# Kernel tuning notes

Hardware: AMD Instinct MI355X
Metric: run time of the kernel (lower is better)

## Reference

```python
import jax, jax.numpy as jnp
import numpy as np

EMBED_DIM = 1024
NUM_HEADS = 16
HEAD_DIM = EMBED_DIM // NUM_HEADS


def setup_inputs() -> dict:
    key = jax.random.key(0)
    ks = jax.random.split(key, 5)
    B, S, D = 2, 2048, EMBED_DIM
    scale_w = 1.0 / np.sqrt(D)
    x = jax.random.normal(ks[0], (B, S, D), dtype=jnp.float32)
    Wq = jax.random.normal(ks[1], (D, D), dtype=jnp.float32) * scale_w
    Wk = jax.random.normal(ks[2], (D, D), dtype=jnp.float32) * scale_w
    Wv = jax.random.normal(ks[3], (D, D), dtype=jnp.float32) * scale_w
    Wo = jax.random.normal(ks[4], (D, D), dtype=jnp.float32) * scale_w
    return {"x": x, "Wq": Wq, "Wk": Wk, "Wv": Wv, "Wo": Wo}


def reference(x, Wq, Wk, Wv, Wo):
    B, S, D = x.shape
    H, Dh = NUM_HEADS, HEAD_DIM
    scale = 1.0 / jnp.sqrt(jnp.asarray(Dh, dtype=x.dtype))

    def split_heads(t):
        return t.reshape(B, S, H, Dh).transpose(0, 2, 1, 3)  # [B,H,S,Dh]

    q = split_heads(x @ Wq)
    k = split_heads(x @ Wk)
    v = split_heads(x @ Wv)

    scores = jnp.einsum("bhqd,bhkd->bhqk", q, k) * scale
    causal = jnp.tril(jnp.ones((S, S), dtype=bool))[None, None]
    scores = jnp.where(causal, scores, jnp.asarray(-1e9, dtype=scores.dtype))
    weights = jax.nn.softmax(scores, axis=-1)
    attn = jnp.einsum("bhqk,bhkd->bhqd", weights, v)
    attn = attn.transpose(0, 2, 1, 3).reshape(B, S, D)
    return attn @ Wo
```

## Files before the change

### kernel.cpp

```cpp
#include <hip/hip_runtime.h>
#include <cstdint>

typedef __bf16 bf16;
typedef __bf16 bf16x2 __attribute__((ext_vector_type(2)));
typedef __bf16 bf16x4 __attribute__((ext_vector_type(4)));
typedef __bf16 bf16x8 __attribute__((ext_vector_type(8)));
typedef float f32x4 __attribute__((ext_vector_type(4)));

constexpr int S = 2048, D = 1024, H = 16, HD = 64, B = 2;
constexpr size_t TSZ = (size_t)B * H * S * HD;

__device__ __forceinline__ f32x4 mfma16(bf16x8 a, bf16x8 b, f32x4 c) {
  return __builtin_amdgcn_mfma_f32_16x16x32_bf16(a, b, c, 0, 0, 0);
}

__device__ __forceinline__ void gl_lds16(const bf16* g, bf16* s) {
  __builtin_amdgcn_global_load_lds((__attribute__((address_space(1))) void*)g,
                                   (__attribute__((address_space(3))) void*)s,
                                   16, 0, 0);
}

__global__ __launch_bounds__(256) void prep_x(const float* __restrict__ x,
                                              bf16* __restrict__ xb) {
  const size_t i = (size_t)blockIdx.x * 256 + threadIdx.x;
  const float4 a = ((const float4*)x)[2 * i];
  const float4 b = ((const float4*)x)[2 * i + 1];
  bf16x8 o = {(bf16)a.x, (bf16)a.y, (bf16)a.z, (bf16)a.w,
              (bf16)b.x, (bf16)b.y, (bf16)b.z, (bf16)b.w};
  *(bf16x8*)&xb[i * 8] = o;
}

__global__ __launch_bounds__(256) void prep_w(const float* __restrict__ W0,
                                              const float* __restrict__ W1,
                                              const float* __restrict__ W2,
                                              const float* __restrict__ W3,
                                              bf16* __restrict__ Wt) {
  __shared__ __align__(16) bf16 Lt[64][68];
  const int z = blockIdx.z;
  const float* W = z == 0 ? W0 : z == 1 ? W1 : z == 2 ? W2 : W3;
  const int k0 = blockIdx.x * 64, n0 = blockIdx.y * 64;
  const int t = threadIdx.x, tr = t >> 4, tc = (t & 15) * 4;
#pragma unroll
  for (int p = 0; p < 4; ++p) {
    const int r = 16 * p + tr;
    const float4 v = *(const float4*)&W[(size_t)(k0 + r) * D + n0 + tc];
    Lt[tc + 0][r] = (bf16)v.x;
    Lt[tc + 1][r] = (bf16)v.y;
    Lt[tc + 2][r] = (bf16)v.z;
    Lt[tc + 3][r] = (bf16)v.w;
  }
  __syncthreads();
#pragma unroll
  for (int p = 0; p < 4; ++p) {
    const int n = 16 * p + tr;
    const bf16x4 o = *(const bf16x4*)&Lt[n][tc];
    *(bf16x4*)&Wt[((size_t)z * D + n0 + n) * D + k0 + tc] = o;
  }
}

template <int MODE>
__global__ __launch_bounds__(256) void gemm_bt(const bf16* __restrict__ A,
                                               const bf16* __restrict__ Bt,
                                               void* __restrict__ Cp) {
  constexpr int K = 1024;
  __shared__ __align__(16) bf16 As[128 * 64];
  __shared__ __align__(16) bf16 Bs[128 * 64];

  const int bid = blockIdx.x, nwg = gridDim.x;
  const int lg = (bid & 7) * (nwg >> 3) + (bid >> 3);
  const int bm = (lg & 31) * 128;
  const int bn = (lg >> 5) * 128;

  const int t = threadIdx.x, l = t & 63, w = t >> 6;
  const int c = l & 15, g = l >> 4, cx = c & 7;
  const int lrow = l >> 3;
  const int srcc = ((l & 7) ^ lrow) << 3;
  const int wm = (w >> 1) * 64, wn = (w & 1) * 64;

  f32x4 acc[4][4] = {};

  for (int kt = 0; kt < K / 64; ++kt) {
    const int k0 = kt * 64;
    __syncthreads();
#pragma unroll
    for (int i = 0; i < 4; ++i) {
      const int ci = i * 4 + w;
      const int row = ci * 8 + lrow;
      gl_lds16(A + (size_t)(bm + row) * K + k0 + srcc, As + ci * 512 + l * 8);
      gl_lds16(Bt + (size_t)(bn + row) * K + k0 + srcc, Bs + ci * 512 + l * 8);
    }
    __syncthreads();

    bf16x8 af[4][2], bfv[4][2];
#pragma unroll
    for (int mi = 0; mi < 4; ++mi) {
      const int row = wm + mi * 16 + c;
#pragma unroll
      for (int kh = 0; kh < 2; ++kh)
        af[mi][kh] = *(const bf16x8*)&As[row * 64 + (((kh * 4 + g) ^ cx) << 3)];
    }
#pragma unroll
    for (int ni = 0; ni < 4; ++ni) {
      const int row = wn + ni * 16 + c;
#pragma unroll
      for (int kh = 0; kh < 2; ++kh)
        bfv[ni][kh] = *(const bf16x8*)&Bs[row * 64 + (((kh * 4 + g) ^ cx) << 3)];
    }
#pragma unroll
    for (int mi = 0; mi < 4; ++mi)
#pragma unroll
      for (int ni = 0; ni < 4; ++ni) {
        acc[mi][ni] = mfma16(af[mi][0], bfv[ni][0], acc[mi][ni]);
        acc[mi][ni] = mfma16(af[mi][1], bfv[ni][1], acc[mi][ni]);
      }
  }

#pragma unroll
  for (int mi = 0; mi < 4; ++mi)
#pragma unroll
    for (int ni = 0; ni < 4; ++ni)
#pragma unroll
      for (int r = 0; r < 4; ++r) {
        const int m = bm + wm + mi * 16 + 4 * g + r;
        const int n = bn + wn + ni * 16 + c;
        const float v = acc[mi][ni][r];
        if constexpr (MODE == 0) {
          const int which = n >> 10, nn = n & 1023;
          const int h = nn >> 6, d = nn & 63;
          const int bb = m >> 11, s = m & 2047;
          ((bf16*)Cp)[which * TSZ + ((((size_t)bb * H + h) * S + s) << 6) + d] =
              (bf16)v;
        } else {
          ((float*)Cp)[(size_t)m * D + n] = v;
        }
      }
}

__global__ __launch_bounds__(256, 4) void attn3(const bf16* __restrict__ Q,
                                                const bf16* __restrict__ Kg,
                                                const bf16* __restrict__ Vg,
                                                bf16* __restrict__ O) {
  __shared__ __align__(16) bf16 Ks[64 * 64];
  __shared__ __align__(16) bf16 Vt[64 * 64];
  __shared__ __align__(16) bf16 Pb[4][16 * 64];

  const int bid = blockIdx.x;
  const int qt = 31 - (bid >> 5);
  const int bh = bid & 31;
  const int t = threadIdx.x, l = t & 63, w = t >> 6;
  const int c = l & 15, g = l >> 4, cx = c & 7;
  const int bb = bh >> 4, h = bh & 15;
  const float SC = 0.18033688011112042f;
  const float THRS = 44.3614195558365f;

  const bf16* Kbase = Kg + (size_t)bh * S * HD;
  const bf16* Vbase = Vg + (size_t)bh * S * HD;

  const int q0 = qt * 64;
  const int qglob = q0 + 16 * w + c;
  const bf16* Qrow = Q + ((size_t)bh * S + qglob) * HD;
  const bf16x8 qf0 = *(const bf16x8*)&Qrow[g * 8];
  const bf16x8 qf1 = *(const bf16x8*)&Qrow[32 + g * 8];

  const int kv0 = t >> 3, dg0 = t & 7;
  const int kv1 = kv0 + 32;
  const int p2 = t & 31, dgv = t >> 5;

  bf16x8 ka0 = *(const bf16x8*)&Kbase[kv0 * 64 + dg0 * 8];
  bf16x8 ka1 = *(const bf16x8*)&Kbase[kv1 * 64 + dg0 * 8];
  bf16x8 va0 = *(const bf16x8*)&Vbase[(2 * p2) * 64 + dgv * 8];
  bf16x8 va1 = *(const bf16x8*)&Vbase[(2 * p2 + 1) * 64 + dgv * 8];

  f32x4 oacc[4] = {};
  float mrun = -1e30f, lrun = 0.f;

  for (int kt = 0; kt <= qt; ++kt) {
    __syncthreads();
    *(bf16x8*)&Ks[kv0 * 64 + ((dg0 ^ (kv0 & 7)) << 3)] = ka0;
    *(bf16x8*)&Ks[kv1 * 64 + ((dg0 ^ (kv1 & 7)) << 3)] = ka1;
#pragma unroll
    for (int i = 0; i < 8; ++i) {
      const int vd = 8 * dgv + i;
      bf16x2 pr2 = {va0[i], va1[i]};
      *(bf16x2*)&Vt[vd * 64 + (((p2 >> 2) ^ i) << 3) + ((p2 & 3) << 1)] = pr2;
    }
    bf16x8 kn0 = ka0, kn1 = ka1, vn0 = va0, vn1 = va1;
    if (kt < qt) {
      const bf16* Kt = Kbase + (size_t)(kt + 1) * 64 * HD;
      const bf16* Vs = Vbase + (size_t)(kt + 1) * 64 * HD;
      kn0 = *(const bf16x8*)&Kt[kv0 * 64 + dg0 * 8];
      kn1 = *(const bf16x8*)&Kt[kv1 * 64 + dg0 * 8];
      vn0 = *(const bf16x8*)&Vs[(2 * p2) * 64 + dgv * 8];
      vn1 = *(const bf16x8*)&Vs[(2 * p2 + 1) * 64 + dgv * 8];
    }
    __syncthreads();

    f32x4 st[4];
    __builtin_amdgcn_s_setprio(1);
#pragma unroll
    for (int ct = 0; ct < 4; ++ct) {
      const int krow = ct * 16 + c;
      const bf16x8 kf0 = *(const bf16x8*)&Ks[krow * 64 + ((g ^ cx) << 3)];
      const bf16x8 kf1 = *(const bf16x8*)&Ks[krow * 64 + (((4 + g) ^ cx) << 3)];
      f32x4 z = {};
      z = mfma16(kf0, qf0, z);
      st[ct] = mfma16(kf1, qf1, z);
    }
    __builtin_amdgcn_s_setprio(0);

    if (kt == qt) {
#pragma unroll
      for (int ct = 0; ct < 4; ++ct)
#pragma unroll
        for (int r = 0; r < 4; ++r)
          if (kt * 64 + ct * 16 + 4 * g + r > qglob) st[ct][r] = -1e30f;
    }

    float mt = st[0][0];
#pragma unroll
    for (int ct = 0; ct < 4; ++ct)
#pragma unroll
      for (int r = 0; r < 4; ++r) mt = fmaxf(mt, st[ct][r]);
    mt = fmaxf(mt, __shfl_xor(mt, 16));
    mt = fmaxf(mt, __shfl_xor(mt, 32));
    if (!__all(mt <= mrun + THRS)) {
      const float mnew = fmaxf(mrun, mt);
      const float fac = __builtin_amdgcn_exp2f((mrun - mnew) * SC);
      lrun *= fac;
#pragma unroll
      for (int ct = 0; ct < 4; ++ct)
#pragma unroll
        for (int r = 0; r < 4; ++r) oacc[ct][r] *= fac;
      mrun = mnew;
    }
    float p[4][4];
    float ps = 0.f;
#pragma unroll
    for (int ct = 0; ct < 4; ++ct)
#pragma unroll
      for (int r = 0; r < 4; ++r) {
        p[ct][r] = __builtin_amdgcn_exp2f((st[ct][r] - mrun) * SC);
        ps += p[ct][r];
      }
    ps += __shfl_xor(ps, 16);
    ps += __shfl_xor(ps, 32);
    lrun += ps;

    bf16* Pw = &Pb[w][0];
#pragma unroll
    for (int ct = 0; ct < 4; ++ct)
#pragma unroll
      for (int pr = 0; pr < 2; ++pr) {
        const int ch = (2 * ct + (g >> 1)) ^ cx;
        bf16x2 pk = {(bf16)p[ct][2 * pr], (bf16)p[ct][2 * pr + 1]};
        *(bf16x2*)&Pw[c * 64 + ch * 8 + (g & 1) * 4 + pr * 2] = pk;
      }
    const bf16x8 pa0 = *(const bf16x8*)&Pw[c * 64 + ((g ^ cx) << 3)];
    const bf16x8 pa1 = *(const bf16x8*)&Pw[c * 64 + (((4 + g) ^ cx) << 3)];

    __builtin_amdgcn_s_setprio(1);
#pragma unroll
    for (int ct = 0; ct < 4; ++ct) {
      const int vrow = ct * 16 + c;
      const bf16x8 vt0 = *(const bf16x8*)&Vt[vrow * 64 + ((g ^ cx) << 3)];
      const bf16x8 vt1 = *(const bf16x8*)&Vt[vrow * 64 + (((4 + g) ^ cx) << 3)];
      oacc[ct] = mfma16(vt0, pa0, oacc[ct]);
      oacc[ct] = mfma16(vt1, pa1, oacc[ct]);
    }
    __builtin_amdgcn_s_setprio(0);

    ka0 = kn0; ka1 = kn1; va0 = vn0; va1 = vn1;
  }

  const float inv = 1.f / lrun;
  bf16* Orow = O + ((size_t)bb * S + qglob) * D + h * 64;
#pragma unroll
  for (int ct = 0; ct < 4; ++ct)
#pragma unroll
    for (int pr = 0; pr < 2; ++pr) {
      bf16x2 pk = {(bf16)(oacc[ct][2 * pr] * inv),
                   (bf16)(oacc[ct][2 * pr + 1] * inv)};
      *(bf16x2*)&Orow[ct * 16 + 4 * g + 2 * pr] = pk;
    }
}

extern "C" void kernel_launch(void* const* d_in, const int* in_sizes, int n_in,
                              void* d_out, int out_size, void* d_ws, size_t ws_size,
                              hipStream_t stream) {
  const float* x  = (const float*)d_in[0];
  const float* Wq = (const float*)d_in[1];
  const float* Wk = (const float*)d_in[2];
  const float* Wv = (const float*)d_in[3];
  const float* Wo = (const float*)d_in[4];
  float* out = (float*)d_out;

  bf16* xb  = (bf16*)d_ws;
  bf16* Wt  = xb + (size_t)B * S * D;
  bf16* QKV = Wt + (size_t)4 * D * D;
  bf16* Ab  = QKV + 3 * TSZ;

  prep_x<<<2048, 256, 0, stream>>>(x, xb);
  prep_w<<<dim3(16, 16, 4), 256, 0, stream>>>(Wq, Wk, Wv, Wo, Wt);
  gemm_bt<0><<<768, 256, 0, stream>>>(xb, Wt, QKV);
  attn3<<<1024, 256, 0, stream>>>(QKV, QKV + TSZ, QKV + 2 * TSZ, Ab);
  gemm_bt<1><<<256, 256, 0, stream>>>(Ab, Wt + (size_t)3 * D * D, out);
}
```

Before: 109.2 us.

## Split KV across wave pairs with paired causal tiles and in-register P

The attention kernel now uses 32-row query tiles, each processed by two head-wave pairs that split every 64-key tile in half, then merges the two partial softmax states through shared memory. Each block handles a short and a long query tile (qp and 63-qp) so causal work per block is balanced. The P fragment is built directly in registers as the MFMA operand, removing the per-wave P staging in shared memory, and V is read with a transposed half-tile layout. The trade-off is an extra LDS merge, two more barriers per phase, and K/V tiles being reloaded for each of the two phases.

```diff
diff --git a/kernel.cpp b/kernel.cpp
--- a/kernel.cpp
+++ b/kernel.cpp
@@ -136,18 +136,19 @@
       }
 }
 
-__global__ __launch_bounds__(256, 4) void attn3(const bf16* __restrict__ Q,
+__global__ __launch_bounds__(256, 4) void attn5(const bf16* __restrict__ Q,
                                                 const bf16* __restrict__ Kg,
                                                 const bf16* __restrict__ Vg,
                                                 bf16* __restrict__ O) {
-  __shared__ __align__(16) bf16 Ks[64 * 64];
-  __shared__ __align__(16) bf16 Vt[64 * 64];
-  __shared__ __align__(16) bf16 Pb[4][16 * 64];
+  __shared__ __align__(16) unsigned char shraw[17408];
+  bf16* Ks = (bf16*)shraw;
+  bf16* Vt = (bf16*)(shraw + 8192);
+  float* X = (float*)shraw;
 
   const int bid = blockIdx.x;
-  const int qt = 31 - (bid >> 5);
-  const int bh = bid & 31;
+  const int qp = bid >> 5, bh = bid & 31;
   const int t = threadIdx.x, l = t & 63, w = t >> 6;
+  const int h2 = w >> 1, pk = w & 1;
   const int c = l & 15, g = l >> 4, cx = c & 7;
   const int bb = bh >> 4, h = bh & 15;
   const float SC = 0.18033688011112042f;
@@ -156,132 +157,139 @@
   const bf16* Kbase = Kg + (size_t)bh * S * HD;
   const bf16* Vbase = Vg + (size_t)bh * S * HD;
 
-  const int q0 = qt * 64;
-  const int qglob = q0 + 16 * w + c;
-  const bf16* Qrow = Q + ((size_t)bh * S + qglob) * HD;
-  const bf16x8 qf0 = *(const bf16x8*)&Qrow[g * 8];
-  const bf16x8 qf1 = *(const bf16x8*)&Qrow[32 + g * 8];
-
-  const int kv0 = t >> 3, dg0 = t & 7;
-  const int kv1 = kv0 + 32;
+  const int kv0 = t >> 3, dg0 = t & 7, kv1 = kv0 + 32;
   const int p2 = t & 31, dgv = t >> 5;
 
-  bf16x8 ka0 = *(const bf16x8*)&Kbase[kv0 * 64 + dg0 * 8];
-  bf16x8 ka1 = *(const bf16x8*)&Kbase[kv1 * 64 + dg0 * 8];
-  bf16x8 va0 = *(const bf16x8*)&Vbase[(2 * p2) * 64 + dgv * 8];
-  bf16x8 va1 = *(const bf16x8*)&Vbase[(2 * p2 + 1) * 64 + dgv * 8];
-
-  f32x4 oacc[4] = {};
-  float mrun = -1e30f, lrun = 0.f;
-
-  for (int kt = 0; kt <= qt; ++kt) {
+  for (int ph = 0; ph < 2; ++ph) {
+    const int qt = ph ? (63 - qp) : qp;
+    const int nT = (qt >> 1) + 1;
+    const int qglob = qt * 32 + 16 * h2 + c;
+
+    const bf16* Qrow = Q + ((size_t)bh * S + qglob) * HD;
+    const bf16x8 qf0 = *(const bf16x8*)&Qrow[g * 8];
+    const bf16x8 qf1 = *(const bf16x8*)&Qrow[32 + g * 8];
+
+    bf16x8 ka0 = *(const bf16x8*)&Kbase[kv0 * 64 + dg0 * 8];
+    bf16x8 ka1 = *(const bf16x8*)&Kbase[kv1 * 64 + dg0 * 8];
+    bf16x8 va0 = *(const bf16x8*)&Vbase[(2 * p2) * 64 + dgv * 8];
+    bf16x8 va1 = *(const bf16x8*)&Vbase[(2 * p2 + 1) * 64 + dgv * 8];
+
+    f32x4 oacc[4] = {};
+    float mrun = -1e30f, lrun = 0.f;
+
+    for (int kt = 0; kt < nT; ++kt) {
+      __syncthreads();
+      *(bf16x8*)&Ks[kv0 * 64 + ((dg0 ^ (kv0 & 7)) << 3)] = ka0;
+      *(bf16x8*)&Ks[kv1 * 64 + ((dg0 ^ (kv1 & 7)) << 3)] = ka1;
+#pragma unroll
+      for (int i = 0; i < 8; ++i) {
+        const int vd = 8 * dgv + i;
+        bf16x2 pr2 = {va0[i], va1[i]};
+        *(bf16x2*)&Vt[vd * 64 + (((p2 >> 2) ^ i) << 3) + ((p2 & 3) << 1)] = pr2;
+      }
+      if (kt + 1 < nT) {
+        const bf16* Kt = Kbase + (size_t)(kt + 1) * 64 * HD;
+        const bf16* Vs = Vbase + (size_t)(kt + 1) * 64 * HD;
+        ka0 = *(const bf16x8*)&Kt[kv0 * 64 + dg0 * 8];
+        ka1 = *(const bf16x8*)&Kt[kv1 * 64 + dg0 * 8];
+        va0 = *(const bf16x8*)&Vs[(2 * p2) * 64 + dgv * 8];
+        va1 = *(const bf16x8*)&Vs[(2 * p2 + 1) * 64 + dgv * 8];
+      }
+      __syncthreads();
+
+      f32x4 st[2];
+      __builtin_amdgcn_s_setprio(1);
+#pragma unroll
+      for (int ct = 0; ct < 2; ++ct) {
+        const int krow = 32 * pk + 16 * ct + c;
+        const bf16x8 kf0 = *(const bf16x8*)&Ks[krow * 64 + ((g ^ cx) << 3)];
+        const bf16x8 kf1 = *(const bf16x8*)&Ks[krow * 64 + (((4 + g) ^ cx) << 3)];
+        f32x4 z = {};
+        z = mfma16(kf0, qf0, z);
+        st[ct] = mfma16(kf1, qf1, z);
+      }
+      __builtin_amdgcn_s_setprio(0);
+
+      if (kt == nT - 1) {
+#pragma unroll
+        for (int ct = 0; ct < 2; ++ct)
+#pragma unroll
+          for (int r = 0; r < 4; ++r)
+            if (kt * 64 + 32 * pk + 16 * ct + 4 * g + r > qglob)
+              st[ct][r] = -3e38f;
+      }
+
+      float mt = st[0][0];
+#pragma unroll
+      for (int ct = 0; ct < 2; ++ct)
+#pragma unroll
+        for (int r = 0; r < 4; ++r) mt = fmaxf(mt, st[ct][r]);
+      mt = fmaxf(mt, __shfl_xor(mt, 16));
+      mt = fmaxf(mt, __shfl_xor(mt, 32));
+      if (!__all(mt <= mrun + THRS)) {
+        const float mnew = fmaxf(mrun, mt);
+        const float fac = __builtin_amdgcn_exp2f((mrun - mnew) * SC);
+        lrun *= fac;
+#pragma unroll
+        for (int q = 0; q < 4; ++q)
+#pragma unroll
+          for (int r = 0; r < 4; ++r) oacc[q][r] *= fac;
+        mrun = mnew;
+      }
+      float p[2][4];
+      float ps = 0.f;
+#pragma unroll
+      for (int ct = 0; ct < 2; ++ct)
+#pragma unroll
+        for (int r = 0; r < 4; ++r) {
+          p[ct][r] = __builtin_amdgcn_exp2f((st[ct][r] - mrun) * SC);
+          ps += p[ct][r];
+        }
+      ps += __shfl_xor(ps, 16);
+      ps += __shfl_xor(ps, 32);
+      lrun += ps;
+
+      const bf16x8 pa = {(bf16)p[0][0], (bf16)p[0][1], (bf16)p[0][2], (bf16)p[0][3],
+                         (bf16)p[1][0], (bf16)p[1][1], (bf16)p[1][2], (bf16)p[1][3]};
+
+      __builtin_amdgcn_s_setprio(1);
+#pragma unroll
+      for (int cp = 0; cp < 4; ++cp) {
+        const int vb = (16 * cp + c) * 64;
+        const bf16x4 lo = *(const bf16x4*)&Vt[vb + ((((pk << 2) + (g >> 1)) ^ cx) << 3) + ((g & 1) << 2)];
+        const bf16x4 hi = *(const bf16x4*)&Vt[vb + ((((pk << 2) + 2 + (g >> 1)) ^ cx) << 3) + ((g & 1) << 2)];
+        const bf16x8 vf = {lo[0], lo[1], lo[2], lo[3], hi[0], hi[1], hi[2], hi[3]};
+        oacc[cp] = mfma16(vf, pa, oacc[cp]);
+      }
+      __builtin_amdgcn_s_setprio(0);
+    }
+
     __syncthreads();
-    *(bf16x8*)&Ks[kv0 * 64 + ((dg0 ^ (kv0 & 7)) << 3)] = ka0;
-    *(bf16x8*)&Ks[kv1 * 64 + ((dg0 ^ (kv1 & 7)) << 3)] = ka1;
-#pragma unroll
-    for (int i = 0; i < 8; ++i) {
-      const int vd = 8 * dgv + i;
-      bf16x2 pr2 = {va0[i], va1[i]};
-      *(bf16x2*)&Vt[vd * 64 + (((p2 >> 2) ^ i) << 3) + ((p2 & 3) << 1)] = pr2;
-    }
-    bf16x8 kn0 = ka0, kn1 = ka1, vn0 = va0, vn1 = va1;
-    if (kt < qt) {
-      const bf16* Kt = Kbase + (size_t)(kt + 1) * 64 * HD;
-      const bf16* Vs = Vbase + (size_t)(kt + 1) * 64 * HD;
-      kn0 = *(const bf16x8*)&Kt[kv0 * 64 + dg0 * 8];
-      kn1 = *(const bf16x8*)&Kt[kv1 * 64 + dg0 * 8];
-      vn0 = *(const bf16x8*)&Vs[(2 * p2) * 64 + dgv * 8];
-      vn1 = *(const bf16x8*)&Vs[(2 * p2 + 1) * 64 + dgv * 8];
-    }
+    float* Xw = X + w * (16 * 68);
+#pragma unroll
+    for (int cp = 0; cp < 4; ++cp)
+      *(f32x4*)&Xw[c * 68 + 16 * cp + 4 * g] = oacc[cp];
+    if (g == 0) { Xw[c * 68 + 64] = mrun; Xw[c * 68 + 65] = lrun; }
     __syncthreads();
-
-    f32x4 st[4];
-    __builtin_amdgcn_s_setprio(1);
-#pragma unroll
-    for (int ct = 0; ct < 4; ++ct) {
-      const int krow = ct * 16 + c;
-      const bf16x8 kf0 = *(const bf16x8*)&Ks[krow * 64 + ((g ^ cx) << 3)];
-      const bf16x8 kf1 = *(const bf16x8*)&Ks[krow * 64 + (((4 + g) ^ cx) << 3)];
-      f32x4 z = {};
-      z = mfma16(kf0, qf0, z);
-      st[ct] = mfma16(kf1, qf1, z);
-    }
-    __builtin_amdgcn_s_setprio(0);
-
-    if (kt == qt) {
-#pragma unroll
-      for (int ct = 0; ct < 4; ++ct)
-#pragma unroll
-        for (int r = 0; r < 4; ++r)
-          if (kt * 64 + ct * 16 + 4 * g + r > qglob) st[ct][r] = -1e30f;
-    }
-
-    float mt = st[0][0];
-#pragma unroll
-    for (int ct = 0; ct < 4; ++ct)
-#pragma unroll
-      for (int r = 0; r < 4; ++r) mt = fmaxf(mt, st[ct][r]);
-    mt = fmaxf(mt, __shfl_xor(mt, 16));
-    mt = fmaxf(mt, __shfl_xor(mt, 32));
-    if (!__all(mt <= mrun + THRS)) {
-      const float mnew = fmaxf(mrun, mt);
-      const float fac = __builtin_amdgcn_exp2f((mrun - mnew) * SC);
-      lrun *= fac;
-#pragma unroll
-      for (int ct = 0; ct < 4; ++ct)
-#pragma unroll
-        for (int r = 0; r < 4; ++r) oacc[ct][r] *= fac;
-      mrun = mnew;
-    }
-    float p[4][4];
-    float ps = 0.f;
-#pragma unroll
-    for (int ct = 0; ct < 4; ++ct)
-#pragma unroll
-      for (int r = 0; r < 4; ++r) {
-        p[ct][r] = __builtin_amdgcn_exp2f((st[ct][r] - mrun) * SC);
-        ps += p[ct][r];
-      }
-    ps += __shfl_xor(ps, 16);
-    ps += __shfl_xor(ps, 32);
-    lrun += ps;
-
-    bf16* Pw = &Pb[w][0];
-#pragma unroll
-    for (int ct = 0; ct < 4; ++ct)
+    const float* Xp = X + (w ^ 1) * (16 * 68);
+    const float m2 = Xp[c * 68 + 64], l2 = Xp[c * 68 + 65];
+    const float mn = fmaxf(mrun, m2);
+    const float f1 = __builtin_amdgcn_exp2f((mrun - mn) * SC);
+    const float f2 = __builtin_amdgcn_exp2f((m2 - mn) * SC);
+    const float linv = 1.f / (lrun * f1 + l2 * f2);
+    bf16* Orow = O + ((size_t)bb * S + qglob) * D + h * 64;
+#pragma unroll
+    for (int j = 0; j < 2; ++j) {
+      const int cp = 2 * pk + j;
+      const f32x4 o2 = *(const f32x4*)&Xp[c * 68 + 16 * cp + 4 * g];
 #pragma unroll
       for (int pr = 0; pr < 2; ++pr) {
-        const int ch = (2 * ct + (g >> 1)) ^ cx;
-        bf16x2 pk = {(bf16)p[ct][2 * pr], (bf16)p[ct][2 * pr + 1]};
-        *(bf16x2*)&Pw[c * 64 + ch * 8 + (g & 1) * 4 + pr * 2] = pk;
-      }
-    const bf16x8 pa0 = *(const bf16x8*)&Pw[c * 64 + ((g ^ cx) << 3)];
-    const bf16x8 pa1 = *(const bf16x8*)&Pw[c * 64 + (((4 + g) ^ cx) << 3)];
-
-    __builtin_amdgcn_s_setprio(1);
-#pragma unroll
-    for (int ct = 0; ct < 4; ++ct) {
-      const int vrow = ct * 16 + c;
-      const bf16x8 vt0 = *(const bf16x8*)&Vt[vrow * 64 + ((g ^ cx) << 3)];
-      const bf16x8 vt1 = *(const bf16x8*)&Vt[vrow * 64 + (((4 + g) ^ cx) << 3)];
-      oacc[ct] = mfma16(vt0, pa0, oacc[ct]);
-      oacc[ct] = mfma16(vt1, pa1, oacc[ct]);
-    }
-    __builtin_amdgcn_s_setprio(0);
-
-    ka0 = kn0; ka1 = kn1; va0 = vn0; va1 = vn1;
+        bf16x2 pkk = {(bf16)((oacc[cp][2 * pr] * f1 + o2[2 * pr] * f2) * linv),
+                      (bf16)((oacc[cp][2 * pr + 1] * f1 + o2[2 * pr + 1] * f2) * linv)};
+        *(bf16x2*)&Orow[16 * cp + 4 * g + 2 * pr] = pkk;
+      }
+    }
   }
-
-  const float inv = 1.f / lrun;
-  bf16* Orow = O + ((size_t)bb * S + qglob) * D + h * 64;
-#pragma unroll
-  for (int ct = 0; ct < 4; ++ct)
-#pragma unroll
-    for (int pr = 0; pr < 2; ++pr) {
-      bf16x2 pk = {(bf16)(oacc[ct][2 * pr] * inv),
-                   (bf16)(oacc[ct][2 * pr + 1] * inv)};
-      *(bf16x2*)&Orow[ct * 16 + 4 * g + 2 * pr] = pk;
-    }
 }
 
 extern "C" void kernel_launch(void* const* d_in, const int* in_sizes, int n_in,
@@ -302,6 +310,6 @@
   prep_x<<<2048, 256, 0, stream>>>(x, xb);
   prep_w<<<dim3(16, 16, 4), 256, 0, stream>>>(Wq, Wk, Wv, Wo, Wt);
   gemm_bt<0><<<768, 256, 0, stream>>>(xb, Wt, QKV);
-  attn3<<<1024, 256, 0, stream>>>(QKV, QKV + TSZ, QKV + 2 * TSZ, Ab);
+  attn5<<<1024, 256, 0, stream>>>(QKV, QKV + TSZ, QKV + 2 * TSZ, Ab);
   gemm_bt<1><<<256, 256, 0, stream>>>(Ab, Wt + (size_t)3 * D * D, out);
 }
```

After: 120.9 us. 1.11x slower.

## Split long causal attention rows across KV halves with a separate merge kernel

Applied to the files above, without the earlier changes.

Query tiles 16-31, which have the longest causal KV ranges, are each split into two blocks that process halves of the KV range. Each block writes unnormalized fp32 partial outputs plus running max and sum to a workspace. A new merge kernel combines the partials and normalizes into the bf16 attention buffer. The launch bound also rises to 6 blocks per CU. The aim is to balance per-block work and raise occupancy, at the cost of an extra kernel launch and fp32 partial-result traffic.

```diff
diff --git a/kernel.cpp b/kernel.cpp
--- a/kernel.cpp
+++ b/kernel.cpp
@@ -136,20 +136,23 @@
       }
 }
 
-__global__ __launch_bounds__(256, 4) void attn3(const bf16* __restrict__ Q,
+__global__ __launch_bounds__(256, 6) void attn6(const bf16* __restrict__ Q,
                                                 const bf16* __restrict__ Kg,
                                                 const bf16* __restrict__ Vg,
-                                                bf16* __restrict__ O) {
+                                                float* __restrict__ Pp) {
   __shared__ __align__(16) bf16 Ks[64 * 64];
   __shared__ __align__(16) bf16 Vt[64 * 64];
   __shared__ __align__(16) bf16 Pb[4][16 * 64];
 
   const int bid = blockIdx.x;
-  const int qt = 31 - (bid >> 5);
-  const int bh = bid & 31;
+  const int bh = bid & 31, e = bid >> 5;
+  int qt, kvA, kvB, half;
+  if (e < 16)      { qt = 31 - e; half = 0; kvA = 0;             kvB = (qt + 2) >> 1; }
+  else if (e < 32) { qt = 47 - e; half = 1; kvA = (qt + 2) >> 1; kvB = qt + 1; }
+  else             { qt = 47 - e; half = 0; kvA = 0;             kvB = qt + 1; }
+
   const int t = threadIdx.x, l = t & 63, w = t >> 6;
   const int c = l & 15, g = l >> 4, cx = c & 7;
-  const int bb = bh >> 4, h = bh & 15;
   const float SC = 0.18033688011112042f;
   const float THRS = 44.3614195558365f;
 
@@ -166,15 +169,17 @@
   const int kv1 = kv0 + 32;
   const int p2 = t & 31, dgv = t >> 5;
 
-  bf16x8 ka0 = *(const bf16x8*)&Kbase[kv0 * 64 + dg0 * 8];
-  bf16x8 ka1 = *(const bf16x8*)&Kbase[kv1 * 64 + dg0 * 8];
-  bf16x8 va0 = *(const bf16x8*)&Vbase[(2 * p2) * 64 + dgv * 8];
-  bf16x8 va1 = *(const bf16x8*)&Vbase[(2 * p2 + 1) * 64 + dgv * 8];
+  const bf16* K0 = Kbase + (size_t)kvA * 64 * HD;
+  const bf16* V0 = Vbase + (size_t)kvA * 64 * HD;
+  bf16x8 ka0 = *(const bf16x8*)&K0[kv0 * 64 + dg0 * 8];
+  bf16x8 ka1 = *(const bf16x8*)&K0[kv1 * 64 + dg0 * 8];
+  bf16x8 va0 = *(const bf16x8*)&V0[(2 * p2) * 64 + dgv * 8];
+  bf16x8 va1 = *(const bf16x8*)&V0[(2 * p2 + 1) * 64 + dgv * 8];
 
   f32x4 oacc[4] = {};
   float mrun = -1e30f, lrun = 0.f;
 
-  for (int kt = 0; kt <= qt; ++kt) {
+  for (int kt = kvA; kt < kvB; ++kt) {
     __syncthreads();
     *(bf16x8*)&Ks[kv0 * 64 + ((dg0 ^ (kv0 & 7)) << 3)] = ka0;
     *(bf16x8*)&Ks[kv1 * 64 + ((dg0 ^ (kv1 & 7)) << 3)] = ka1;
@@ -185,7 +190,7 @@
       *(bf16x2*)&Vt[vd * 64 + (((p2 >> 2) ^ i) << 3) + ((p2 & 3) << 1)] = pr2;
     }
     bf16x8 kn0 = ka0, kn1 = ka1, vn0 = va0, vn1 = va1;
-    if (kt < qt) {
+    if (kt + 1 < kvB) {
       const bf16* Kt = Kbase + (size_t)(kt + 1) * 64 * HD;
       const bf16* Vs = Vbase + (size_t)(kt + 1) * 64 * HD;
       kn0 = *(const bf16x8*)&Kt[kv0 * 64 + dg0 * 8];
@@ -272,16 +277,33 @@
     ka0 = kn0; ka1 = kn1; va0 = vn0; va1 = vn1;
   }
 
-  const float inv = 1.f / lrun;
-  bf16* Orow = O + ((size_t)bb * S + qglob) * D + h * 64;
+  float* Pr = Pp + ((((size_t)bh * 32 + qt) * 2 + half) * 64 + 16 * w + c) * 68;
 #pragma unroll
   for (int ct = 0; ct < 4; ++ct)
-#pragma unroll
-    for (int pr = 0; pr < 2; ++pr) {
-      bf16x2 pk = {(bf16)(oacc[ct][2 * pr] * inv),
-                   (bf16)(oacc[ct][2 * pr + 1] * inv)};
-      *(bf16x2*)&Orow[ct * 16 + 4 * g + 2 * pr] = pk;
-    }
+    *(f32x4*)&Pr[16 * ct + 4 * g] = oacc[ct];
+  if (g == 0) { Pr[64] = mrun; Pr[65] = lrun; }
+}
+
+__global__ __launch_bounds__(256) void attn_merge(const float* __restrict__ Pp,
+                                                  bf16* __restrict__ Ab) {
+  const float SC = 0.18033688011112042f;
+  const int gid = blockIdx.x * 4 + (threadIdx.x >> 6);
+  const int bh = gid >> 11, s = gid & 2047;
+  const int lane = threadIdx.x & 63;
+  const int qt = s >> 6, row = s & 63;
+  const float* r0 = Pp + ((((size_t)bh * 32 + qt) * 2 + 0) * 64 + row) * 68;
+  float o = r0[lane];
+  float m = r0[64], l = r0[65];
+  if (qt >= 16) {
+    const float* r1 = r0 + 64 * 68;
+    const float o1 = r1[lane], m1 = r1[64], l1 = r1[65];
+    const float mn = fmaxf(m, m1);
+    const float f0 = exp2f((m - mn) * SC), f1 = exp2f((m1 - mn) * SC);
+    o = o * f0 + o1 * f1;
+    l = l * f0 + l1 * f1;
+  }
+  const int bb = bh >> 4, h = bh & 15;
+  Ab[((size_t)bb * S + s) * D + h * 64 + lane] = (bf16)(o / l);
 }
 
 extern "C" void kernel_launch(void* const* d_in, const int* in_sizes, int n_in,
@@ -298,10 +320,12 @@
   bf16* Wt  = xb + (size_t)B * S * D;
   bf16* QKV = Wt + (size_t)4 * D * D;
   bf16* Ab  = QKV + 3 * TSZ;
+  float* Pp = (float*)(Ab + TSZ);
 
   prep_x<<<2048, 256, 0, stream>>>(x, xb);
   prep_w<<<dim3(16, 16, 4), 256, 0, stream>>>(Wq, Wk, Wv, Wo, Wt);
   gemm_bt<0><<<768, 256, 0, stream>>>(xb, Wt, QKV);
-  attn3<<<1024, 256, 0, stream>>>(QKV, QKV + TSZ, QKV + 2 * TSZ, Ab);
+  attn6<<<1536, 256, 0, stream>>>(QKV, QKV + TSZ, QKV + 2 * TSZ, Pp);
+  attn_merge<<<16384, 256, 0, stream>>>(Pp, Ab);
   gemm_bt<1><<<256, 256, 0, stream>>>(Ab, Wt + (size_t)3 * D * D, out);
 }
```

Measured after the change: 138.7 us. +27.1%, slower.

## Process two KV tiles per barrier and stage K via direct global-to-LDS loads

Applied to the files above, without the earlier changes.

The attention kernel now handles 128 keys per outer iteration, with two 64-key sub-steps. This halves the number of block-wide barrier pairs and LDS staging rounds. K is loaded straight into swizzled LDS with global_load_lds instead of going through registers, so its register prefetch is dropped. V keeps a register prefetch that now spans two tiles. The risk is that K's load latency is no longer hidden behind the previous iteration's compute, and the doubled LDS footprint and extra V registers may reduce occupancy.

```diff
diff --git a/kernel.cpp b/kernel.cpp
--- a/kernel.cpp
+++ b/kernel.cpp
@@ -136,12 +136,12 @@
       }
 }
 
-__global__ __launch_bounds__(256, 4) void attn3(const bf16* __restrict__ Q,
+__global__ __launch_bounds__(256, 4) void attn7(const bf16* __restrict__ Q,
                                                 const bf16* __restrict__ Kg,
                                                 const bf16* __restrict__ Vg,
                                                 bf16* __restrict__ O) {
-  __shared__ __align__(16) bf16 Ks[64 * 64];
-  __shared__ __align__(16) bf16 Vt[64 * 64];
+  __shared__ __align__(16) bf16 Ks[128 * 64];
+  __shared__ __align__(16) bf16 Vt[64 * 128];
   __shared__ __align__(16) bf16 Pb[4][16 * 64];
 
   const int bid = blockIdx.x;
@@ -162,114 +162,127 @@
   const bf16x8 qf0 = *(const bf16x8*)&Qrow[g * 8];
   const bf16x8 qf1 = *(const bf16x8*)&Qrow[32 + g * 8];
 
-  const int kv0 = t >> 3, dg0 = t & 7;
-  const int kv1 = kv0 + 32;
+  const int lr = l >> 3;
+  const int ksrc = ((l & 7) ^ lr) << 3;
   const int p2 = t & 31, dgv = t >> 5;
 
-  bf16x8 ka0 = *(const bf16x8*)&Kbase[kv0 * 64 + dg0 * 8];
-  bf16x8 ka1 = *(const bf16x8*)&Kbase[kv1 * 64 + dg0 * 8];
   bf16x8 va0 = *(const bf16x8*)&Vbase[(2 * p2) * 64 + dgv * 8];
   bf16x8 va1 = *(const bf16x8*)&Vbase[(2 * p2 + 1) * 64 + dgv * 8];
+  bf16x8 va2 = *(const bf16x8*)&Vbase[(64 + 2 * p2) * 64 + dgv * 8];
+  bf16x8 va3 = *(const bf16x8*)&Vbase[(65 + 2 * p2) * 64 + dgv * 8];
 
   f32x4 oacc[4] = {};
   float mrun = -1e30f, lrun = 0.f;
-
-  for (int kt = 0; kt <= qt; ++kt) {
+  const int nP = (qt >> 1) + 1;
+
+  for (int it = 0; it < nP; ++it) {
+    const int kt0 = 2 * it;
+    const bool hasB = (kt0 + 1 <= qt);
     __syncthreads();
-    *(bf16x8*)&Ks[kv0 * 64 + ((dg0 ^ (kv0 & 7)) << 3)] = ka0;
-    *(bf16x8*)&Ks[kv1 * 64 + ((dg0 ^ (kv1 & 7)) << 3)] = ka1;
+
+    const bf16* Kp = Kbase + (size_t)kt0 * 64 * HD;
+#pragma unroll
+    for (int i = 0; i < 4; ++i) {
+      const int ci = i * 4 + w;
+      gl_lds16(Kp + (size_t)(ci * 8 + lr) * 64 + ksrc, Ks + ci * 512 + l * 8);
+    }
 #pragma unroll
     for (int i = 0; i < 8; ++i) {
       const int vd = 8 * dgv + i;
-      bf16x2 pr2 = {va0[i], va1[i]};
-      *(bf16x2*)&Vt[vd * 64 + (((p2 >> 2) ^ i) << 3) + ((p2 & 3) << 1)] = pr2;
-    }
-    bf16x8 kn0 = ka0, kn1 = ka1, vn0 = va0, vn1 = va1;
-    if (kt < qt) {
-      const bf16* Kt = Kbase + (size_t)(kt + 1) * 64 * HD;
-      const bf16* Vs = Vbase + (size_t)(kt + 1) * 64 * HD;
-      kn0 = *(const bf16x8*)&Kt[kv0 * 64 + dg0 * 8];
-      kn1 = *(const bf16x8*)&Kt[kv1 * 64 + dg0 * 8];
-      vn0 = *(const bf16x8*)&Vs[(2 * p2) * 64 + dgv * 8];
-      vn1 = *(const bf16x8*)&Vs[(2 * p2 + 1) * 64 + dgv * 8];
+      bf16x2 pa = {va0[i], va1[i]};
+      bf16x2 pb = {va2[i], va3[i]};
+      const int sl0 = (p2 >> 2) ^ i;
+      *(bf16x2*)&Vt[vd * 128 + (sl0 << 3) + ((p2 & 3) << 1)] = pa;
+      *(bf16x2*)&Vt[vd * 128 + ((8 | sl0) << 3) + ((p2 & 3) << 1)] = pb;
+    }
+    if (it + 1 < nP) {
+      const bf16* Vn = Vbase + (size_t)(kt0 + 2) * 64 * HD;
+      va0 = *(const bf16x8*)&Vn[(2 * p2) * 64 + dgv * 8];
+      va1 = *(const bf16x8*)&Vn[(2 * p2 + 1) * 64 + dgv * 8];
+      va2 = *(const bf16x8*)&Vn[(64 + 2 * p2) * 64 + dgv * 8];
+      va3 = *(const bf16x8*)&Vn[(65 + 2 * p2) * 64 + dgv * 8];
     }
     __syncthreads();
 
-    f32x4 st[4];
-    __builtin_amdgcn_s_setprio(1);
-#pragma unroll
-    for (int ct = 0; ct < 4; ++ct) {
-      const int krow = ct * 16 + c;
-      const bf16x8 kf0 = *(const bf16x8*)&Ks[krow * 64 + ((g ^ cx) << 3)];
-      const bf16x8 kf1 = *(const bf16x8*)&Ks[krow * 64 + (((4 + g) ^ cx) << 3)];
-      f32x4 z = {};
-      z = mfma16(kf0, qf0, z);
-      st[ct] = mfma16(kf1, qf1, z);
-    }
-    __builtin_amdgcn_s_setprio(0);
-
-    if (kt == qt) {
+    const int nSub = hasB ? 2 : 1;
+    for (int sub = 0; sub < nSub; ++sub) {
+      f32x4 st[4];
+      __builtin_amdgcn_s_setprio(1);
+#pragma unroll
+      for (int ct = 0; ct < 4; ++ct) {
+        const int krow = sub * 64 + ct * 16 + c;
+        const bf16x8 kf0 = *(const bf16x8*)&Ks[krow * 64 + ((g ^ cx) << 3)];
+        const bf16x8 kf1 = *(const bf16x8*)&Ks[krow * 64 + (((4 + g) ^ cx) << 3)];
+        f32x4 z = {};
+        z = mfma16(kf0, qf0, z);
+        st[ct] = mfma16(kf1, qf1, z);
+      }
+      __builtin_amdgcn_s_setprio(0);
+
+      if (kt0 + sub == qt) {
+#pragma unroll
+        for (int ct = 0; ct < 4; ++ct)
+#pragma unroll
+          for (int r = 0; r < 4; ++r)
+            if ((kt0 + sub) * 64 + ct * 16 + 4 * g + r > qglob)
+              st[ct][r] = -1e30f;
+      }
+
+      float mt = st[0][0];
 #pragma unroll
       for (int ct = 0; ct < 4; ++ct)
 #pragma unroll
-        for (int r = 0; r < 4; ++r)
-          if (kt * 64 + ct * 16 + 4 * g + r > qglob) st[ct][r] = -1e30f;
-    }
-
-    float mt = st[0][0];
-#pragma unroll
-    for (int ct = 0; ct < 4; ++ct)
-#pragma unroll
-      for (int r = 0; r < 4; ++r) mt = fmaxf(mt, st[ct][r]);
-    mt = fmaxf(mt, __shfl_xor(mt, 16));
-    mt = fmaxf(mt, __shfl_xor(mt, 32));
-    if (!__all(mt <= mrun + THRS)) {
-      const float mnew = fmaxf(mrun, mt);
-      const float fac = __builtin_amdgcn_exp2f((mrun - mnew) * SC);
-      lrun *= fac;
+        for (int r = 0; r < 4; ++r) mt = fmaxf(mt, st[ct][r]);
+      mt = fmaxf(mt, __shfl_xor(mt, 16));
+      mt = fmaxf(mt, __shfl_xor(mt, 32));
+      if (!__all(mt <= mrun + THRS)) {
+        const float mnew = fmaxf(mrun, mt);
+        const float fac = __builtin_amdgcn_exp2f((mrun - mnew) * SC);
+        lrun *= fac;
+#pragma unroll
+        for (int ct = 0; ct < 4; ++ct)
+#pragma unroll
+          for (int r = 0; r < 4; ++r) oacc[ct][r] *= fac;
+        mrun = mnew;
+      }
+      float p[4][4];
+      float ps = 0.f;
 #pragma unroll
       for (int ct = 0; ct < 4; ++ct)
 #pragma unroll
-        for (int r = 0; r < 4; ++r) oacc[ct][r] *= fac;
-      mrun = mnew;
-    }
-    float p[4][4];
-    float ps = 0.f;
-#pragma unroll
-    for (int ct = 0; ct < 4; ++ct)
-#pragma unroll
-      for (int r = 0; r < 4; ++r) {
-        p[ct][r] = __builtin_amdgcn_exp2f((st[ct][r] - mrun) * SC);
-        ps += p[ct][r];
-      }
-    ps += __shfl_xor(ps, 16);
-    ps += __shfl_xor(ps, 32);
-    lrun += ps;
-
-    bf16* Pw = &Pb[w][0];
-#pragma unroll
-    for (int ct = 0; ct < 4; ++ct)
-#pragma unroll
-      for (int pr = 0; pr < 2; ++pr) {
-        const int ch = (2 * ct + (g >> 1)) ^ cx;
-        bf16x2 pk = {(bf16)p[ct][2 * pr], (bf16)p[ct][2 * pr + 1]};
-        *(bf16x2*)&Pw[c * 64 + ch * 8 + (g & 1) * 4 + pr * 2] = pk;
-      }
-    const bf16x8 pa0 = *(const bf16x8*)&Pw[c * 64 + ((g ^ cx) << 3)];
-    const bf16x8 pa1 = *(const bf16x8*)&Pw[c * 64 + (((4 + g) ^ cx) << 3)];
-
-    __builtin_amdgcn_s_setprio(1);
-#pragma unroll
-    for (int ct = 0; ct < 4; ++ct) {
-      const int vrow = ct * 16 + c;
-      const bf16x8 vt0 = *(const bf16x8*)&Vt[vrow * 64 + ((g ^ cx) << 3)];
-      const bf16x8 vt1 = *(const bf16x8*)&Vt[vrow * 64 + (((4 + g) ^ cx) << 3)];
-      oacc[ct] = mfma16(vt0, pa0, oacc[ct]);
-      oacc[ct] = mfma16(vt1, pa1, oacc[ct]);
-    }
-    __builtin_amdgcn_s_setprio(0);
-
-    ka0 = kn0; ka1 = kn1; va0 = vn0; va1 = vn1;
+        for (int r = 0; r < 4; ++r) {
+          p[ct][r] = __builtin_amdgcn_exp2f((st[ct][r] - mrun) * SC);
+          ps += p[ct][r];
+        }
+      ps += __shfl_xor(ps, 16);
+      ps += __shfl_xor(ps, 32);
+      lrun += ps;
+
+      bf16* Pw = &Pb[w][0];
+#pragma unroll
+      for (int ct = 0; ct < 4; ++ct)
+#pragma unroll
+        for (int pr = 0; pr < 2; ++pr) {
+          const int ch = (2 * ct + (g >> 1)) ^ cx;
+          bf16x2 pk = {(bf16)p[ct][2 * pr], (bf16)p[ct][2 * pr + 1]};
+          *(bf16x2*)&Pw[c * 64 + ch * 8 + (g & 1) * 4 + pr * 2] = pk;
+        }
+      const bf16x8 pa0 = *(const bf16x8*)&Pw[c * 64 + ((g ^ cx) << 3)];
+      const bf16x8 pa1 = *(const bf16x8*)&Pw[c * 64 + (((4 + g) ^ cx) << 3)];
+
+      __builtin_amdgcn_s_setprio(1);
+#pragma unroll
+      for (int ct = 0; ct < 4; ++ct) {
+        const int vrow = ct * 16 + c;
+        const bf16x8 vt0 =
+            *(const bf16x8*)&Vt[vrow * 128 + (((sub * 8 + g) ^ cx) << 3)];
+        const bf16x8 vt1 =
+            *(const bf16x8*)&Vt[vrow * 128 + (((sub * 8 + 4 + g) ^ cx) << 3)];
+        oacc[ct] = mfma16(vt0, pa0, oacc[ct]);
+        oacc[ct] = mfma16(vt1, pa1, oacc[ct]);
+      }
+      __builtin_amdgcn_s_setprio(0);
+    }
   }
 
   const float inv = 1.f / lrun;
@@ -302,6 +315,6 @@
   prep_x<<<2048, 256, 0, stream>>>(x, xb);
   prep_w<<<dim3(16, 16, 4), 256, 0, stream>>>(Wq, Wk, Wv, Wo, Wt);
   gemm_bt<0><<<768, 256, 0, stream>>>(xb, Wt, QKV);
-  attn3<<<1024, 256, 0, stream>>>(QKV, QKV + TSZ, QKV + 2 * TSZ, Ab);
+  attn7<<<1024, 256, 0, stream>>>(QKV, QKV + TSZ, QKV + 2 * TSZ, Ab);
   gemm_bt<1><<<256, 256, 0, stream>>>(Ab, Wt + (size_t)3 * D * D, out);
 }
```

Measured after the change: 121.2 us. 1.11x slower.
